# Kernel tuning notes

Measured on AMD Instinct MI355X. Metric: run time of the kernel, lower is better.

The kernel has to match this reference:

```python
import jax, jax.numpy as jnp
import numpy as np

DIM = 512
HEADS = 8
DIM_HEAD = 64
INNER = HEADS * DIM_HEAD  # 512
HIDDEN = 512 * 4          # mlp_dim * expansion
EPS = 1e-5
SCALE = DIM_HEAD ** -0.5


def layernorm(x, w, b):
    mu = jnp.mean(x, axis=-1, keepdims=True)
    var = jnp.var(x, axis=-1, keepdims=True)
    return (x - mu) * jax.lax.rsqrt(var + EPS) * w + b


def setup_inputs() -> dict:
    key = jax.random.key(0)
    ks = jax.random.split(key, 12)
    B, P, N = 2, 8, 1024  # P must equal HEADS (axis-swap bug in original rearrange)
    s = lambda k, shape, fan: jax.random.normal(k, shape, jnp.float32) * (fan ** -0.5)
    return {
        "x": jax.random.normal(ks[0], (B, P, N, DIM), jnp.float32),
        "ln0_w": jnp.ones((DIM,), jnp.float32),
        "ln0_b": jnp.zeros((DIM,), jnp.float32),
        "ln1_w": jnp.ones((DIM,), jnp.float32),
        "ln1_b": jnp.zeros((DIM,), jnp.float32),
        "w_qkv": s(ks[1], (DIM, 3 * INNER), DIM),
        "w_o": s(ks[2], (INNER, DIM), INNER),
        "b_o": jnp.zeros((DIM,), jnp.float32),
        "w1": s(ks[3], (DIM, HIDDEN), DIM),
        "b1": jnp.zeros((HIDDEN,), jnp.float32),
        "w2": s(ks[4], (HIDDEN, DIM), HIDDEN),
        "b2": jnp.zeros((DIM,), jnp.float32),
    }


def reference(x, ln0_w, ln0_b, ln1_w, ln1_b, w_qkv, w_o, b_o, w1, b1, w2, b2):
    B, P, N, _ = x.shape
    x = layernorm(x, ln0_w, ln0_b)  # outer block norm

    # ---- VisionAttention ----
    h = layernorm(x, ln1_w, ln1_b)
    qkv = h @ w_qkv                                    # [B,P,N,3*INNER]
    q, k, v = jnp.split(qkv, 3, axis=-1)
    def to_heads(t):  # [B,P,N,H*D] -> [B,H,P,N,D]
        return t.reshape(B, P, N, HEADS, DIM_HEAD).transpose(0, 3, 1, 2, 4)
    q, k, v = to_heads(q), to_heads(k), to_heads(v)
    dots = jnp.einsum("bhpnd,bhpmd->bhpnm", q, k) * SCALE  # full NxN scores
    attn = jax.nn.softmax(dots, axis=-1)
    out = jnp.einsum("bhpnm,bhpmd->bhpnd", attn, v)        # [B,H,P,N,D]
    # Faithful to buggy rearrange 'b p h n d -> b p n (h d)': swaps H and P axes.
    out = out.transpose(0, 1, 3, 2, 4).reshape(B, HEADS, N, P * DIM_HEAD)
    out = out @ w_o + b_o                                  # [B,H,N,DIM]
    x = out + x  # residual (valid because P == HEADS)

    # ---- MLP ----
    m = jax.nn.gelu(x @ w1 + b1, approximate=False) @ w2 + b2
    return m + x
```

## Files before the change

### kernel.cpp

```cpp
#include <hip/hip_runtime.h>
#include <hip/hip_bf16.h>
#include <math.h>

#define DIMV 512
#define NTOK 16384
#define NSEQ 1024
#define HEADSV 8
#define PPV 8
#define DHEAD 64
#define QKVW 1536
#define HIDV 2048
#define SC2 0.18033688011112042f

typedef unsigned short ushort;
typedef unsigned int uint;
typedef __attribute__((ext_vector_type(8))) short short8;
typedef __attribute__((ext_vector_type(8))) unsigned short ushort8;
typedef __attribute__((ext_vector_type(4))) unsigned short ushortx4;
typedef __attribute__((ext_vector_type(4))) float floatx4;

__device__ __forceinline__ float bf2f(ushort u){
  union { unsigned int i; float f; } c; c.i = ((unsigned int)u) << 16; return c.f;
}
__device__ __forceinline__ ushort f2bf(float f){
  union { float f; unsigned int i; } c; c.f = f;
  unsigned int u = c.i + 0x7fffu + ((c.i >> 16) & 1u);
  return (ushort)(u >> 16);
}
__device__ __forceinline__ void async_copy16(const void* gptr, void* lptr){
  __builtin_amdgcn_global_load_lds((const __attribute__((address_space(1))) void*)gptr,
                                   (__attribute__((address_space(3))) void*)lptr, 16, 0, 0);
}
__device__ __forceinline__ float fast_gelu(float x){
  float u = x * (2.3022084f + 0.1029435f * x * x);
  return x * __builtin_amdgcn_rcpf(1.f + exp2f(-u));
}

__device__ __forceinline__ void wave_reduce2(float& a, float& b){
  #pragma unroll
  for (int off = 32; off > 0; off >>= 1){
    a += __shfl_down(a, off, 64);
    b += __shfl_down(b, off, 64);
  }
}

__device__ __forceinline__ void wtrans_body(const float* __restrict__ W,
    __hip_bfloat16* __restrict__ Wt, int K, int N, int bx, int by, int t,
    float* tile ){
  int bn = bx * 32, bk = by * 32;
  int tx = t & 31, ty = t >> 5;
  #pragma unroll
  for (int i = 0; i < 32; i += 8)
    tile[(ty + i) * 33 + tx] = W[(size_t)(bk + ty + i) * N + bn + tx];
  __syncthreads();
  #pragma unroll
  for (int i = 0; i < 32; i += 8)
    Wt[(size_t)(bn + ty + i) * K + bk + tx] = __float2bfloat16(tile[tx * 33 + ty + i]);
}

__global__ __launch_bounds__(256) void prep_kernel(const float* __restrict__ x,
    const float* __restrict__ w0, const float* __restrict__ b0,
    const float* __restrict__ w1ln, const float* __restrict__ b1ln,
    __hip_bfloat16* __restrict__ x1, __hip_bfloat16* __restrict__ h,
    const float* __restrict__ wqkv, __hip_bfloat16* __restrict__ wqkvT,
    const float* __restrict__ wo,   __hip_bfloat16* __restrict__ woT,
    const float* __restrict__ w1,   __hip_bfloat16* __restrict__ w1T,
    const float* __restrict__ w2,   __hip_bfloat16* __restrict__ w2T){
  __shared__ float smem[32 * 33];
  int bid = blockIdx.x;
  int t = threadIdx.x;
  if (bid >= NTOK){
    int r = bid - NTOK;
    if (r < 768)        wtrans_body(wqkv, wqkvT, 512, 1536, r % 48, r / 48, t, smem);
    else if (r < 1024){ r -= 768;  wtrans_body(wo, woT, 512, 512,  r % 16, r / 16, t, smem); }
    else if (r < 2048){ r -= 1024; wtrans_body(w1, w1T, 512, 2048, r % 64, r / 64, t, smem); }
    else             { r -= 2048; wtrans_body(w2, w2T, 2048, 512, r % 16, r / 16, t, smem); }
    return;
  }
  float* sm = smem;
  size_t row = bid;
  const float2* xr = (const float2*)(x + row * DIMV);
  float2 v = xr[t];
  float s = v.x + v.y;
  float sq = v.x * v.x + v.y * v.y;
  wave_reduce2(s, sq);
  int wid = t >> 6, lane = t & 63;
  if (lane == 0){ sm[wid] = s; sm[8 + wid] = sq; }
  __syncthreads();
  s  = sm[0] + sm[1] + sm[2] + sm[3];
  sq = sm[8] + sm[9] + sm[10] + sm[11];
  float mu = s * (1.f / DIMV);
  float var = sq * (1.f / DIMV) - mu * mu;
  float r = rsqrtf(var + 1e-5f);
  float2 ww = ((const float2*)w0)[t];
  float2 bb = ((const float2*)b0)[t];
  float2 y;
  y.x = (v.x - mu) * r * ww.x + bb.x;
  y.y = (v.y - mu) * r * ww.y + bb.y;
  ushort2 xb; xb.x = f2bf(y.x); xb.y = f2bf(y.y);
  ((ushort2*)(x1 + row * DIMV))[t] = xb;
  float s2 = y.x + y.y, sq2 = y.x * y.x + y.y * y.y;
  wave_reduce2(s2, sq2);
  __syncthreads();
  if (lane == 0){ sm[wid] = s2; sm[8 + wid] = sq2; }
  __syncthreads();
  s2  = sm[0] + sm[1] + sm[2] + sm[3];
  sq2 = sm[8] + sm[9] + sm[10] + sm[11];
  float mu2 = s2 * (1.f / DIMV);
  float var2 = sq2 * (1.f / DIMV) - mu2 * mu2;
  float r2 = rsqrtf(var2 + 1e-5f);
  float2 w1v = ((const float2*)w1ln)[t];
  float2 b1v = ((const float2*)b1ln)[t];
  float hx = (y.x - mu2) * r2 * w1v.x + b1v.x;
  float hy = (y.y - mu2) * r2 * w1v.y + b1v.y;
  ushort2 hb; hb.x = f2bf(hx); hb.y = f2bf(hy);
  ((ushort2*)(h + row * DIMV))[t] = hb;
}

template<int SWAP>
__global__ __launch_bounds__(256) void gemm_mfma(
    const __hip_bfloat16* __restrict__ A,
    const __hip_bfloat16* __restrict__ Bt,
    const float* __restrict__ bias,
    const __hip_bfloat16* __restrict__ Rb,
    float* __restrict__ Cf,
    __hip_bfloat16* __restrict__ Cb,
    ushort* __restrict__ vt,
    int M, int N, int K, int gx, int dogelu)
{
  __shared__ __hip_bfloat16 As[2][128 * 32];
  __shared__ __hip_bfloat16 Bs[2][128 * 32];
  int tid = threadIdx.x;
  int w = tid >> 6, l = tid & 63;

  int bid = blockIdx.x;
  int xcd = bid & 7, idx = bid >> 3;
  int xl = idx % gx, yl = idx / gx;
  size_t bm = (size_t)(xcd * 16 + yl) * 128;
  size_t bn = (size_t)xl * 128;
  int wm = (w & 1) * 64, wn = (w >> 1) * 64;

  int srow = w * 16 + (l >> 2);
  int scol = (l & 3) * 8;
  const __hip_bfloat16* Ag0 = A + (bm + srow) * K + scol;
  const __hip_bfloat16* Ag1 = A + (bm + 64 + srow) * K + scol;
  const __hip_bfloat16* Bg0 = Bt + (bn + srow) * K + scol;
  const __hip_bfloat16* Bg1 = Bt + (bn + 64 + srow) * K + scol;
  int lo = srow * 32 + scol;

  floatx4 acc[4][4] = {};
  int fm = l & 15;
  int quad = l >> 4;
  int fq = quad * 8;

  async_copy16(Ag0, &As[0][lo]);
  async_copy16(Ag1, &As[0][lo + 64 * 32]);
  async_copy16(Bg0, &Bs[0][lo]);
  async_copy16(Bg1, &Bs[0][lo + 64 * 32]);

  int nk = K >> 5;
  for (int it = 0; it < nk; ++it){
    int cur = it & 1;
    if (it + 1 < nk){
      int nxt = cur ^ 1;
      int k0 = (it + 1) << 5;
      async_copy16(Ag0 + k0, &As[nxt][lo]);
      async_copy16(Ag1 + k0, &As[nxt][lo + 64 * 32]);
      async_copy16(Bg0 + k0, &Bs[nxt][lo]);
      async_copy16(Bg1 + k0, &Bs[nxt][lo + 64 * 32]);
      asm volatile("s_waitcnt vmcnt(4)\n\ts_barrier" ::: "memory");
    } else {
      asm volatile("s_waitcnt vmcnt(0)\n\ts_barrier" ::: "memory");
    }
    const __hip_bfloat16* Ab = As[cur];
    const __hip_bfloat16* Bb = Bs[cur];
    short8 af[4], bf[4];
    #pragma unroll
    for (int i = 0; i < 4; i++){
      af[i] = *(const short8*)&Ab[(wm + i * 16 + fm) * 32 + fq];
      bf[i] = *(const short8*)&Bb[(wn + i * 16 + fm) * 32 + fq];
    }
    #pragma unroll
    for (int mi = 0; mi < 4; mi++)
      #pragma unroll
      for (int ni = 0; ni < 4; ni++){
        if (SWAP)
          acc[mi][ni] = __builtin_amdgcn_mfma_f32_16x16x32_bf16(bf[ni], af[mi], acc[mi][ni], 0, 0, 0);
        else
          acc[mi][ni] = __builtin_amdgcn_mfma_f32_16x16x32_bf16(af[mi], bf[ni], acc[mi][ni], 0, 0, 0);
      }
    asm volatile("s_waitcnt lgkmcnt(0)\n\ts_barrier" ::: "memory");
  }

  int rq = quad * 4;
  if (SWAP){
    #pragma unroll
    for (int mi = 0; mi < 4; mi++){
      size_t row = bm + wm + mi * 16 + fm;
      size_t rbase = row * (size_t)N + bn + wn + rq;
      #pragma unroll
      for (int ni = 0; ni < 4; ni++){
        size_t idx2 = rbase + ni * 16;
        floatx4 v = acc[mi][ni];
        if (bias){
          floatx4 bv = *(const floatx4*)(bias + bn + wn + ni * 16 + rq);
          #pragma unroll
          for (int r2 = 0; r2 < 4; r2++) v[r2] += bv[r2];
        }
        if (dogelu){
          #pragma unroll
          for (int r2 = 0; r2 < 4; r2++) v[r2] = fast_gelu(v[r2]);
        }
        if (Rb){
          ushortx4 rb = *(const ushortx4*)((const ushort*)Rb + idx2);
          #pragma unroll
          for (int r2 = 0; r2 < 4; r2++) v[r2] += bf2f(rb[r2]);
        }
        if (Cb){
          ushortx4 ob;
          #pragma unroll
          for (int r2 = 0; r2 < 4; r2++) ob[r2] = f2bf(v[r2]);
          *(ushortx4*)((ushort*)Cb + idx2) = ob;
        } else {
          *(floatx4*)(Cf + idx2) = v;
        }
      }
    }
  } else {
    if (vt && bn >= 1024){
      int b = (int)(bm >> 13), p = (int)((bm >> 10) & 7);
      int n0 = (int)(bm & 1023) + wm + rq;
      int cbase = (int)bn + wn - 1024;
      #pragma unroll
      for (int ni = 0; ni < 4; ni++){
        int cc = cbase + ni * 16 + fm;
        int hh = cc >> 6, dd = cc & 63;
        ushort* vdst = vt + ((size_t)((b * 8 + hh) * 8 + p)) * 65536 + (size_t)dd * 1024;
        #pragma unroll
        for (int mi = 0; mi < 4; mi++){
          ushortx4 v4;
          v4[0] = f2bf(acc[mi][ni][0]); v4[1] = f2bf(acc[mi][ni][1]);
          v4[2] = f2bf(acc[mi][ni][2]); v4[3] = f2bf(acc[mi][ni][3]);
          *(ushortx4*)(vdst + n0 + mi * 16) = v4;
        }
      }
    } else if (Cb){
      float scl = (vt && bn < 512) ? SC2 : 1.f;
      #pragma unroll
      for (int ni = 0; ni < 4; ni++){
        size_t col = bn + wn + ni * 16 + fm;
        float bv = bias ? bias[col] : 0.f;
        #pragma unroll
        for (int mi = 0; mi < 4; mi++){
          #pragma unroll
          for (int r2 = 0; r2 < 4; r2++){
            size_t row = bm + wm + mi * 16 + rq + r2;
            float v = acc[mi][ni][r2];
            if (vt) v *= scl;
            v += bv;
            if (dogelu) v = fast_gelu(v);
            size_t idx2 = row * N + col;
            if (Rb) v += bf2f(((const ushort*)Rb)[idx2]);
            ((ushort*)Cb)[idx2] = f2bf(v);
          }
        }
      }
    } else {
      #pragma unroll
      for (int ni = 0; ni < 4; ni++){
        size_t col = bn + wn + ni * 16 + fm;
        float bv = bias ? bias[col] : 0.f;
        #pragma unroll
        for (int mi = 0; mi < 4; mi++){
          #pragma unroll
          for (int r2 = 0; r2 < 4; r2++){
            size_t row = bm + wm + mi * 16 + rq + r2;
            float v = acc[mi][ni][r2] + bv;
            if (dogelu) v = fast_gelu(v);
            size_t idx2 = row * N + col;
            if (Rb) v += bf2f(((const ushort*)Rb)[idx2]);
            Cf[idx2] = v;
          }
        }
      }
    }
  }
}

__global__ __launch_bounds__(256, 4) void attn_mfma(const __hip_bfloat16* __restrict__ qkvp,
                                                    const ushort* __restrict__ vt,
                                                    __hip_bfloat16* __restrict__ outp){
  __shared__ ushort Ks[2][64 * 64];
  __shared__ ushort Vs[2][64 * 64];
  __shared__ ushort Ps[4][32 * 32];
  int tid = threadIdx.x;
  int w = tid >> 6, l = tid & 63;
  int r15 = l & 15, quad = l >> 4, fq = quad * 8;
  int slice = blockIdx.x & 127;
  int qc = blockIdx.x >> 7;
  int b = slice >> 6, hh = (slice >> 3) & 7, p = slice & 7;
  const ushort* base = (const ushort*)qkvp + (size_t)(b * PPV + p) * NSEQ * QKVW;
  const ushort* kb = base + 512 + hh * DHEAD;
  const ushort* vb = vt + (size_t)slice * 65536;

  int s0 = w * 64 + l, s1 = 256 + w * 64 + l;
  int row0 = s0 >> 3, row1 = s1 >> 3;
  int gc0 = (s0 & 7) ^ (row0 & 7), gc1 = (s1 & 7) ^ (row1 & 7);
  const ushort* kp0 = kb + (size_t)row0 * QKVW + gc0 * 8;
  const ushort* kp1 = kb + (size_t)row1 * QKVW + gc1 * 8;
  const ushort* vp0 = vb + (size_t)row0 * 1024 + gc0 * 8;
  const ushort* vp1 = vb + (size_t)row1 * 1024 + gc1 * 8;

  async_copy16(kp0, &Ks[0][s0 * 8]);
  async_copy16(kp1, &Ks[0][s1 * 8]);
  async_copy16(vp0, &Vs[0][s0 * 8]);
  async_copy16(vp1, &Vs[0][s1 * 8]);

  int q0 = qc * 128 + w * 32;
  short8 qf[2][2];
  #pragma unroll
  for (int mi = 0; mi < 2; mi++)
    #pragma unroll
    for (int kk = 0; kk < 2; kk++)
      qf[mi][kk] = *(const short8*)(base + (size_t)(q0 + mi * 16 + r15) * QKVW + hh * DHEAD + kk * 32 + fq);

  floatx4 o[2][4] = {};
  floatx4 lacc[2] = {};
  short8 ones;
  #pragma unroll
  for (int j = 0; j < 8; j++) ones[j] = (short)0x3F80;

  int sw = r15 & 7;
  int swp = (r15 & 3) << 3;
  ushort* PsW = Ps[w];

  for (int it = 0; it < NSEQ / 64; ++it){
    int cur = it & 1;
    if (it + 1 < NSEQ / 64){
      int nxt = cur ^ 1;
      kp0 += 64 * QKVW; kp1 += 64 * QKVW; vp0 += 64; vp1 += 64;
      async_copy16(kp0, &Ks[nxt][s0 * 8]);
      async_copy16(kp1, &Ks[nxt][s1 * 8]);
      async_copy16(vp0, &Vs[nxt][s0 * 8]);
      async_copy16(vp1, &Vs[nxt][s1 * 8]);
      asm volatile("s_waitcnt vmcnt(4)\n\ts_barrier" ::: "memory");
    } else {
      asm volatile("s_waitcnt vmcnt(0)\n\ts_barrier" ::: "memory");
    }
    const ushort* Kb = Ks[cur];
    const ushort* Vb = Vs[cur];

    short8 pf[2][2];
    #pragma unroll
    for (int kk = 0; kk < 2; kk++){
      #pragma unroll
      for (int nn = 0; nn < 2; nn++){
        int ni = kk * 2 + nn;
        int rb2 = (ni * 16 + r15) * 64;
        short8 kf0 = *(const short8*)&Kb[rb2 + (quad ^ sw) * 8];
        short8 kf1 = *(const short8*)&Kb[rb2 + ((4 + quad) ^ sw) * 8];
        floatx4 sA = {}, sB = {};
        sA = __builtin_amdgcn_mfma_f32_16x16x32_bf16(kf0, qf[0][0], sA, 0, 0, 0);
        sA = __builtin_amdgcn_mfma_f32_16x16x32_bf16(kf1, qf[0][1], sA, 0, 0, 0);
        sB = __builtin_amdgcn_mfma_f32_16x16x32_bf16(kf0, qf[1][0], sB, 0, 0, 0);
        sB = __builtin_amdgcn_mfma_f32_16x16x32_bf16(kf1, qf[1][1], sB, 0, 0, 0);
        int wc = (nn * 16 + quad * 4) ^ swp;
        union { float f; uint u; } e0, e1, e2, e3;
        uint2 pk;
        e0.f = exp2f(sA[0]); e1.f = exp2f(sA[1]);
        e2.f = exp2f(sA[2]); e3.f = exp2f(sA[3]);
        pk.x = __builtin_amdgcn_perm(e1.u, e0.u, 0x07060302u);
        pk.y = __builtin_amdgcn_perm(e3.u, e2.u, 0x07060302u);
        *(uint2*)&PsW[r15 * 32 + wc] = pk;
        e0.f = exp2f(sB[0]); e1.f = exp2f(sB[1]);
        e2.f = exp2f(sB[2]); e3.f = exp2f(sB[3]);
        pk.x = __builtin_amdgcn_perm(e1.u, e0.u, 0x07060302u);
        pk.y = __builtin_amdgcn_perm(e3.u, e2.u, 0x07060302u);
        *(uint2*)&PsW[(16 + r15) * 32 + wc] = pk;
      }
      asm volatile("s_waitcnt lgkmcnt(0)" ::: "memory");
      pf[0][kk] = *(const short8*)&PsW[r15 * 32 + (fq ^ swp)];
      pf[1][kk] = *(const short8*)&PsW[(16 + r15) * 32 + (fq ^ swp)];
      asm volatile("s_waitcnt lgkmcnt(0)" ::: "memory");
    }

    #pragma unroll
    for (int mi = 0; mi < 2; mi++)
      #pragma unroll
      for (int kk = 0; kk < 2; kk++)
        lacc[mi] = __builtin_amdgcn_mfma_f32_16x16x32_bf16(ones, pf[mi][kk], lacc[mi], 0, 0, 0);

    #pragma unroll
    for (int dj = 0; dj < 4; dj++){
      int d = dj * 16 + r15;
      short8 vf0 = *(const short8*)&Vb[d * 64 + ((quad) ^ sw) * 8];
      short8 vf1 = *(const short8*)&Vb[d * 64 + ((4 + quad) ^ sw) * 8];
      #pragma unroll
      for (int mi = 0; mi < 2; mi++){
        o[mi][dj] = __builtin_amdgcn_mfma_f32_16x16x32_bf16(vf0, pf[mi][0], o[mi][dj], 0, 0, 0);
        o[mi][dj] = __builtin_amdgcn_mfma_f32_16x16x32_bf16(vf1, pf[mi][1], o[mi][dj], 0, 0, 0);
      }
    }
    asm volatile("s_waitcnt lgkmcnt(0)\n\ts_barrier" ::: "memory");
  }

  #pragma unroll
  for (int mi = 0; mi < 2; mi++){
    float inv = __builtin_amdgcn_rcpf(lacc[mi][0]);
    size_t n = q0 + mi * 16 + r15;
    ushort* orow = (ushort*)outp + ((size_t)((b * HEADSV + hh) * NSEQ + n)) * DIMV + p * DHEAD + quad * 4;
    #pragma unroll
    for (int dj = 0; dj < 4; dj++){
      ushortx4 ov;
      #pragma unroll
      for (int r = 0; r < 4; r++) ov[r] = f2bf(o[mi][dj][r] * inv);
      *(ushortx4*)(orow + dj * 16) = ov;
    }
  }
}

extern "C" void kernel_launch(void* const* d_in, const int* in_sizes, int n_in,
                              void* d_out, int out_size, void* d_ws, size_t ws_size,
                              hipStream_t stream){
  (void)in_sizes; (void)n_in; (void)out_size; (void)ws_size;
  const float* x    = (const float*)d_in[0];
  const float* lw0  = (const float*)d_in[1];
  const float* lb0  = (const float*)d_in[2];
  const float* lw1  = (const float*)d_in[3];
  const float* lb1  = (const float*)d_in[4];
  const float* wqkv = (const float*)d_in[5];
  const float* wo   = (const float*)d_in[6];
  const float* bo   = (const float*)d_in[7];
  const float* w1   = (const float*)d_in[8];
  const float* b1   = (const float*)d_in[9];
  const float* w2   = (const float*)d_in[10];
  const float* b2   = (const float*)d_in[11];
  float* out = (float*)d_out;
  char* ws = (char*)d_ws;
  const size_t MB = 1024 * 1024;

  __hip_bfloat16* x1b  = (__hip_bfloat16*)(ws);
  ushort* vtbuf        = (ushort*)(ws + 32 * MB);
  __hip_bfloat16* x2b  = (__hip_bfloat16*)(ws + 64 * MB);
  __hip_bfloat16* wqkvT= (__hip_bfloat16*)(ws + 80 * MB);
  __hip_bfloat16* woT  = (__hip_bfloat16*)(ws + 82 * MB);
  __hip_bfloat16* w1T  = (__hip_bfloat16*)(ws + 83 * MB);
  __hip_bfloat16* w2T  = (__hip_bfloat16*)(ws + 85 * MB);
  __hip_bfloat16* hB   = (__hip_bfloat16*)(ws + 88 * MB);
  __hip_bfloat16* attnB= hB;
  __hip_bfloat16* qkvB = (__hip_bfloat16*)(ws + 104 * MB);
  __hip_bfloat16* tB   = (__hip_bfloat16*)(ws + 88 * MB);

  prep_kernel<<<NTOK + 3072, 256, 0, stream>>>(
      x, lw0, lb0, lw1, lb1, x1b, hB,
      wqkv, wqkvT, wo, woT, w1, w1T, w2, w2T);

  gemm_mfma<0><<<(QKVW / 128) * 128, 256, 0, stream>>>(
      hB, wqkvT, nullptr, nullptr, nullptr, qkvB, vtbuf,
      NTOK, QKVW, DIMV, QKVW / 128, 0);

  attn_mfma<<<1024, 256, 0, stream>>>(qkvB, vtbuf, attnB);

  gemm_mfma<1><<<(DIMV / 128) * 128, 256, 0, stream>>>(
      attnB, woT, bo, x1b, nullptr, x2b, nullptr,
      NTOK, DIMV, DIMV, DIMV / 128, 0);

  gemm_mfma<1><<<(HIDV / 128) * 128, 256, 0, stream>>>(
      x2b, w1T, b1, nullptr, nullptr, tB, nullptr,
      NTOK, HIDV, DIMV, HIDV / 128, 1);

  gemm_mfma<1><<<(DIMV / 128) * 128, 256, 0, stream>>>(
      tB, w2T, b2, x2b, out, nullptr, nullptr,
      NTOK, DIMV, HIDV, DIMV / 128, 0);
}
```

Measured before the change: 372.7 us.

## Triple-buffer GEMM LDS with swizzle and single barrier per k-step

The GEMM kernel moves from double to triple LDS buffering and prefetches two k-tiles ahead. This lets it drop the trailing lgkmcnt wait and barrier, so each iteration has one barrier. It also XOR-swizzles the 16-byte column chunks by row to cut LDS bank conflicts on fragment reads. The attention kernel is restructured the same way: it waits once at the top of the loop before issuing the next K/V prefetch, removing the second barrier per iteration. The extra LDS buffer raises shared memory use per block, which may limit occupancy.

```diff
diff --git a/kernel.cpp b/kernel.cpp
--- a/kernel.cpp
+++ b/kernel.cpp
@@ -128,8 +128,8 @@
     ushort* __restrict__ vt,
     int M, int N, int K, int gx, int dogelu)
 {
-  __shared__ __hip_bfloat16 As[2][128 * 32];
-  __shared__ __hip_bfloat16 Bs[2][128 * 32];
+  __shared__ __hip_bfloat16 As[3][128 * 32];
+  __shared__ __hip_bfloat16 Bs[3][128 * 32];
   int tid = threadIdx.x;
   int w = tid >> 6, l = tid & 63;
 
@@ -141,44 +141,51 @@
   int wm = (w & 1) * 64, wn = (w >> 1) * 64;
 
   int srow = w * 16 + (l >> 2);
-  int scol = (l & 3) * 8;
-  const __hip_bfloat16* Ag0 = A + (bm + srow) * K + scol;
-  const __hip_bfloat16* Ag1 = A + (bm + 64 + srow) * K + scol;
-  const __hip_bfloat16* Bg0 = Bt + (bn + srow) * K + scol;
-  const __hip_bfloat16* Bg1 = Bt + (bn + 64 + srow) * K + scol;
-  int lo = srow * 32 + scol;
+  int gcs = ((l & 3) ^ (srow & 3)) * 8;
+  const __hip_bfloat16* Ag0 = A + (bm + srow) * K + gcs;
+  const __hip_bfloat16* Ag1 = A + (bm + 64 + srow) * K + gcs;
+  const __hip_bfloat16* Bg0 = Bt + (bn + srow) * K + gcs;
+  const __hip_bfloat16* Bg1 = Bt + (bn + 64 + srow) * K + gcs;
+  int lo = srow * 32 + (l & 3) * 8;
 
   floatx4 acc[4][4] = {};
   int fm = l & 15;
   int quad = l >> 4;
-  int fq = quad * 8;
-
+  int cs = fm & 3;
+
+  int nk = K >> 5;
   async_copy16(Ag0, &As[0][lo]);
   async_copy16(Ag1, &As[0][lo + 64 * 32]);
   async_copy16(Bg0, &Bs[0][lo]);
   async_copy16(Bg1, &Bs[0][lo + 64 * 32]);
-
-  int nk = K >> 5;
+  if (nk > 1){
+    async_copy16(Ag0 + 32, &As[1][lo]);
+    async_copy16(Ag1 + 32, &As[1][lo + 64 * 32]);
+    async_copy16(Bg0 + 32, &Bs[1][lo]);
+    async_copy16(Bg1 + 32, &Bs[1][lo + 64 * 32]);
+  }
+
+  int rb = 0;
   for (int it = 0; it < nk; ++it){
-    int cur = it & 1;
-    if (it + 1 < nk){
-      int nxt = cur ^ 1;
-      int k0 = (it + 1) << 5;
-      async_copy16(Ag0 + k0, &As[nxt][lo]);
-      async_copy16(Ag1 + k0, &As[nxt][lo + 64 * 32]);
-      async_copy16(Bg0 + k0, &Bs[nxt][lo]);
-      async_copy16(Bg1 + k0, &Bs[nxt][lo + 64 * 32]);
+    if (it + 1 < nk)
       asm volatile("s_waitcnt vmcnt(4)\n\ts_barrier" ::: "memory");
-    } else {
+    else
       asm volatile("s_waitcnt vmcnt(0)\n\ts_barrier" ::: "memory");
-    }
-    const __hip_bfloat16* Ab = As[cur];
-    const __hip_bfloat16* Bb = Bs[cur];
+    if (it + 2 < nk){
+      int wb = rb >= 1 ? rb - 1 : 2;
+      int k0 = (it + 2) << 5;
+      async_copy16(Ag0 + k0, &As[wb][lo]);
+      async_copy16(Ag1 + k0, &As[wb][lo + 64 * 32]);
+      async_copy16(Bg0 + k0, &Bs[wb][lo]);
+      async_copy16(Bg1 + k0, &Bs[wb][lo + 64 * 32]);
+    }
+    const __hip_bfloat16* Ab = As[rb];
+    const __hip_bfloat16* Bb = Bs[rb];
     short8 af[4], bf[4];
     #pragma unroll
     for (int i = 0; i < 4; i++){
-      af[i] = *(const short8*)&Ab[(wm + i * 16 + fm) * 32 + fq];
-      bf[i] = *(const short8*)&Bb[(wn + i * 16 + fm) * 32 + fq];
+      af[i] = *(const short8*)&Ab[(wm + i * 16 + fm) * 32 + ((quad ^ cs) * 8)];
+      bf[i] = *(const short8*)&Bb[(wn + i * 16 + fm) * 32 + ((quad ^ cs) * 8)];
     }
     #pragma unroll
     for (int mi = 0; mi < 4; mi++)
@@ -189,7 +196,7 @@
         else
           acc[mi][ni] = __builtin_amdgcn_mfma_f32_16x16x32_bf16(af[mi], bf[ni], acc[mi][ni], 0, 0, 0);
       }
-    asm volatile("s_waitcnt lgkmcnt(0)\n\ts_barrier" ::: "memory");
+    rb = rb < 2 ? rb + 1 : 0;
   }
 
   int rq = quad * 4;
@@ -212,9 +219,9 @@
           for (int r2 = 0; r2 < 4; r2++) v[r2] = fast_gelu(v[r2]);
         }
         if (Rb){
-          ushortx4 rb = *(const ushortx4*)((const ushort*)Rb + idx2);
-          #pragma unroll
-          for (int r2 = 0; r2 < 4; r2++) v[r2] += bf2f(rb[r2]);
+          ushortx4 rbv = *(const ushortx4*)((const ushort*)Rb + idx2);
+          #pragma unroll
+          for (int r2 = 0; r2 < 4; r2++) v[r2] += bf2f(rbv[r2]);
         }
         if (Cb){
           ushortx4 ob;
@@ -336,6 +343,7 @@
 
   for (int it = 0; it < NSEQ / 64; ++it){
     int cur = it & 1;
+    asm volatile("s_waitcnt vmcnt(0)\n\ts_barrier" ::: "memory");
     if (it + 1 < NSEQ / 64){
       int nxt = cur ^ 1;
       kp0 += 64 * QKVW; kp1 += 64 * QKVW; vp0 += 64; vp1 += 64;
@@ -343,9 +351,6 @@
       async_copy16(kp1, &Ks[nxt][s1 * 8]);
       async_copy16(vp0, &Vs[nxt][s0 * 8]);
       async_copy16(vp1, &Vs[nxt][s1 * 8]);
-      asm volatile("s_waitcnt vmcnt(4)\n\ts_barrier" ::: "memory");
-    } else {
-      asm volatile("s_waitcnt vmcnt(0)\n\ts_barrier" ::: "memory");
     }
     const ushort* Kb = Ks[cur];
     const ushort* Vb = Vs[cur];
@@ -401,7 +406,6 @@
         o[mi][dj] = __builtin_amdgcn_mfma_f32_16x16x32_bf16(vf1, pf[mi][1], o[mi][dj], 0, 0, 0);
       }
     }
-    asm volatile("s_waitcnt lgkmcnt(0)\n\ts_barrier" ::: "memory");
   }
 
   #pragma unroll
```

Measured after the change: 366.8 us. About the same (-1.6%).
